# Kernel optimization log

Measured on AMD Instinct MI355X. Metric: run time of the kernel, lower is better.

Reference implementation:

```python
import jax, jax.numpy as jnp
import numpy as np

NS = 33  # segments per image: id 0 = background, 1..32 = objects (fixed max-object count)
EPS_GN = 1e-5


def conv2d(x, w, b, pad):
    y = jax.lax.conv_general_dilated(x, w, window_strides=(1, 1),
                                     padding=[(pad, pad), (pad, pad)],
                                     dimension_numbers=('NCHW', 'OIHW', 'NCHW'))
    return y + b[None, :, None, None]


def group_norm(x, gamma, beta, groups):
    B, C, H, W = x.shape
    xg = x.reshape(B, groups, C // groups, H, W)
    mu = xg.mean((2, 3, 4), keepdims=True)
    var = xg.var((2, 3, 4), keepdims=True)
    xn = ((xg - mu) / jnp.sqrt(var + EPS_GN)).reshape(B, C, H, W)
    return xn * gamma[None, :, None, None] + beta[None, :, None, None]


def setup_inputs() -> dict:
    key = jax.random.key(0)
    ks = jax.random.split(key, 10)
    B, Cf, H, W = 4, 512, 128, 128
    std = 0.01
    inp = {
        'x': jax.random.normal(ks[0], (B, Cf, H, W), jnp.float32),
        'masks': jax.random.randint(ks[1], (B, H, W), 0, NS).astype(jnp.int32),
        # coord_conv: Conv2d(2, 64, 1)
        'w_coord': jax.random.normal(ks[2], (64, 2, 1, 1), jnp.float32) * std,
        'b_coord': jnp.zeros((64,), jnp.float32),
        # encoder convs + groupnorms
        'w1': jax.random.normal(ks[3], (256, Cf + 64, 3, 3), jnp.float32) * std,
        'b1': jnp.zeros((256,), jnp.float32),
        'g1': jnp.ones((256,), jnp.float32), 'bt1': jnp.zeros((256,), jnp.float32),
        'w2': jax.random.normal(ks[4], (128, 256, 3, 3), jnp.float32) * std,
        'b2': jnp.zeros((128,), jnp.float32),
        'g2': jnp.ones((128,), jnp.float32), 'bt2': jnp.zeros((128,), jnp.float32),
        'w3': jax.random.normal(ks[5], (64, 128, 3, 3), jnp.float32) * std,
        'b3': jnp.zeros((64,), jnp.float32),
        'g3': jnp.ones((64,), jnp.float32), 'bt3': jnp.zeros((64,), jnp.float32),
        # heads (1x1 convs on pooled [64] vectors == tiny matmuls)
        'w_box': jax.random.normal(ks[6], (7, 64, 1, 1), jnp.float32) * std,
        'b_box': jnp.zeros((7,), jnp.float32),
        'w_conf': jax.random.normal(ks[7], (1, 64, 1, 1), jnp.float32) * std,
        'b_conf': jnp.zeros((1,), jnp.float32),
    }
    return inp


def reference(x, masks, w_coord, b_coord, w1, b1, g1, bt1, w2, b2, g2, bt2,
              w3, b3, g3, bt3, w_box, b_box, w_conf, b_conf):
    B, _, H, W = x.shape
    # coordinate grid: channels are [grid_x, grid_y]
    gy, gx = jnp.meshgrid(jnp.arange(H), jnp.arange(W), indexing='ij')
    grid = jnp.stack([gx, gy], axis=0).astype(x.dtype)            # [2,H,W]
    grid = jnp.broadcast_to(grid[None], (B, 2, H, W))
    grid_feats = jax.nn.relu(conv2d(grid, w_coord, b_coord, 0))   # [B,64,H,W]

    h = jnp.concatenate([x, grid_feats], axis=1)                  # [B,576,H,W]
    h = jax.nn.relu(group_norm(conv2d(h, w1, b1, 1), g1, bt1, 8))
    h = jax.nn.relu(group_norm(conv2d(h, w2, b2, 1), g2, bt2, 4))
    h = jax.nn.relu(group_norm(conv2d(h, w3, b3, 1), g3, bt3, 4))  # [B,64,H,W]

    # per-(image, object-id) masked mean pooling via segment_sum
    C = h.shape[1]
    flat = h.transpose(0, 2, 3, 1).reshape(-1, C)                 # [B*H*W, 64]
    seg = (jnp.arange(B, dtype=jnp.int32)[:, None] * NS
           + masks.reshape(B, -1)).reshape(-1)                    # [B*H*W]
    sums = jax.ops.segment_sum(flat, seg, num_segments=B * NS).reshape(B, NS, C)
    counts = jax.ops.segment_sum(jnp.ones_like(seg, jnp.float32), seg,
                                 num_segments=B * NS).reshape(B, NS, 1)
    # drop background segment 0; safe divide matches the <1e-4 skip (empty slots -> 0 pooled)
    pooled = sums[:, 1:] / jnp.maximum(counts[:, 1:], 1e-4)       # [B,32,64]

    boxes = jnp.einsum('boc,kc->bok', pooled, w_box.reshape(7, C)) + b_box   # [B,32,7]
    scores = jnp.einsum('boc,c->bo', pooled, w_conf.reshape(C)) + b_conf[0]  # [B,32]
    return boxes, scores
```

## Files before the change

### kernel.cpp

```cpp
#include <hip/hip_runtime.h>

typedef unsigned short u16;
typedef unsigned int u32;
typedef __bf16 bf16x8 __attribute__((ext_vector_type(8)));
typedef float f32x4 __attribute__((ext_vector_type(4)));

__device__ __forceinline__ u16 f2bf(float f) {
  u32 u = __float_as_uint(f);
  u += 0x7fffu + ((u >> 16) & 1u);
  return (u16)(u >> 16);
}
__device__ __forceinline__ float bf2f(u16 h) {
  return __uint_as_float(((u32)h) << 16);
}

#define GLD_LDS16(g, l)                                                        \
  __builtin_amdgcn_global_load_lds(                                            \
      (__attribute__((address_space(1))) void*)(g),                            \
      (__attribute__((address_space(3))) void*)(l), 16, 0, 0)

__global__ __launch_bounds__(256) void prep_k(
    float* smallb, u16* in1, u16* in2, u16* in3, const float* __restrict__ w1,
    u16* __restrict__ wp1, const float* __restrict__ w2, u16* __restrict__ wp2,
    const float* __restrict__ w3, u16* __restrict__ wp3,
    const float* __restrict__ x, const float* __restrict__ wcd,
    const float* __restrict__ bcd) {
  const int bid = blockIdx.x;
  const int t = threadIdx.x;
  __shared__ u16 tile[128 * 65];
  __shared__ float swc[128], sbc[64];

  if (bid < 83) {
    if (bid < 35) {
      int i = bid * 256 + t;
      if (i < 8708) smallb[i] = 0.f;
      return;
    }
    u16* buf;
    int C, sub;
    if (bid < 51)      { buf = in1; C = 576; sub = bid - 35; }
    else if (bid < 67) { buf = in2; C = 256; sub = bid - 51; }
    else               { buf = in3; C = 128; sub = bid - 67; }
    int b = sub >> 2, s = sub & 3;
    int npx = (s < 2) ? 130 : 128;
    u32* base = (u32*)(buf + (size_t)b * 130 * 130 * C);
    int C2 = C >> 1;
    int total = npx * C2;
    for (int i = t; i < total; i += 256) {
      int p = i / C2, r = i - p * C2;
      int y, xx;
      if (s == 0)      { y = 0;     xx = p; }
      else if (s == 1) { y = 129;   xx = p; }
      else if (s == 2) { y = p + 1; xx = 0; }
      else             { y = p + 1; xx = 129; }
      base[(y * 130 + xx) * C2 + r] = 0u;
    }
    return;
  }
  if (bid < 6707) {
    int rel = bid - 83;
    const float* src;
    u16* dst;
    int CIN, COUT, total, base;
    if (rel < 5184)      { src = w1; dst = wp1; CIN = 576; COUT = 256; total = 1327104; base = rel; }
    else if (rel < 6336) { src = w2; dst = wp2; CIN = 256; COUT = 128; total = 294912;  base = rel - 5184; }
    else                 { src = w3; dst = wp3; CIN = 128; COUT = 64;  total = 73728;   base = rel - 6336; }
    int idx = base * 256 + t;
    if (idx >= total) return;
    int kc = idx & 31;
    int n = (idx >> 5) % COUT;
    int q = idx / (32 * COUT);
    int dydx = q % 9, cb = q / 9;
    dst[idx] = f2bf(src[((size_t)n * CIN + cb * 32 + kc) * 9 + dydx]);
    return;
  }
  const int tb = bid - 6707;
  const int b = tb >> 8, h = (tb >> 1) & 127, half = tb & 1;
  const int w0 = half * 64;
  if (t < 128) swc[t] = wcd[t];
  else if (t < 192) sbc[t - 128] = bcd[t - 128];
  const int w = t & 63;
  const int cg = t >> 6;
  const float* xb = x + (((size_t)b * 512) * 128 + h) * 128 + w0 + w;
  u16* ob = in1 + ((size_t)(b * 130 + h + 1) * 130 + (w0 + 1)) * 576;
#pragma unroll 1
  for (int cc = 0; cc < 4; ++cc) {
    const int c0 = cc * 128;
#pragma unroll
    for (int j = 0; j < 32; ++j) {
      int cl = j * 4 + cg;
      tile[cl * 65 + w] = f2bf(xb[(size_t)(c0 + cl) * 16384]);
    }
    __syncthreads();
#pragma unroll
    for (int k = 0; k < 4; ++k) {
      int idx = k * 256 + t;
      int ww = idx >> 4, c8 = (idx & 15) * 8;
      union { uint4 u; u16 s[8]; } o;
#pragma unroll
      for (int i = 0; i < 8; ++i) o.s[i] = tile[(c8 + i) * 65 + ww];
      *(uint4*)(ob + (size_t)ww * 576 + c0 + c8) = o.u;
    }
    __syncthreads();
  }
  const int px = t >> 2, cq = (t & 3) * 16;
  const float fw = (float)(w0 + px), fh = (float)h;
  u16* gp = ob + (size_t)px * 576 + 512 + cq;
#pragma unroll
  for (int j = 0; j < 2; ++j) {
    union { uint4 u; u16 s[8]; } o;
#pragma unroll
    for (int i = 0; i < 8; ++i) {
      int c = cq + j * 8 + i;
      float v = swc[2 * c] * fw + swc[2 * c + 1] * fh + sbc[c];
      o.s[i] = f2bf(fmaxf(v, 0.f));
    }
    *(uint4*)(gp + j * 8) = o.u;
  }
}

template <int CIN, int COUT, int BN, bool NORM>
__global__ __launch_bounds__(256) void conv3x3_k(
    const u16* __restrict__ in, const u16* __restrict__ wp,
    const float* __restrict__ bias, u16* __restrict__ out, int Hp, int Wp,
    int opy, int opx, float* __restrict__ stats, int gsLog2, int nG,
    const float* __restrict__ inStats, const float* __restrict__ inGamma,
    const float* __restrict__ inBeta, int inGsLog2, int inNG) {
  constexpr int CB = CIN / 32;
  constexpr int WN = BN / 2;
  constexpr int NT = WN / 16;
  constexpr int ROWCH = 520;
  constexpr int NCH = 3 * ROWCH;
  constexpr int BUFE = 3 * 130 * 32;
  static_assert(BN == 128 || BN == 64, "");
  __shared__ u16 As3[2 * BUFE];
  __shared__ float redS[8], redQ[8];
  __shared__ float la[NORM ? CIN : 1], lb[NORM ? CIN : 1];

  const int t = threadIdx.x;
  const int L = gridDim.x;
  const int work = (blockIdx.x & 7) * (L >> 3) + (blockIdx.x >> 3);
  const int xt = work >> 9;
  const int rem = work & 511;
  const int b = rem >> 7, h = rem & 127;
  const int n0 = xt * BN;

  const int lane = t & 63, wv = t >> 6;
  const int wm = wv & 1, wn = wv >> 1;
  const int ln = lane & 15, lq = lane >> 4;

  if (t < 8) { redS[t] = 0.f; redQ[t] = 0.f; }
  if (NORM) {
    const float invCnt = 1.f / (16384.f * 32.f);
    for (int i = t; i < CIN; i += 256) {
      int g = i >> inGsLog2;
      float mean = inStats[b * inNG + g] * invCnt;
      float m2 = inStats[4 * inNG + b * inNG + g] * invCnt;
      float rstd = rsqrtf(m2 - mean * mean + 1e-5f);
      float a = inGamma[i] * rstd;
      la[i] = a;
      lb[i] = inBeta[i] - mean * a;
    }
  }

  f32x4 acc[4][NT];
  const f32x4 zero = {0.f, 0.f, 0.f, 0.f};
#pragma unroll
  for (int i = 0; i < 4; ++i)
#pragma unroll
    for (int j = 0; j < NT; ++j) acc[i][j] = zero;

  const u16* inb = in + ((size_t)b * 130 + h) * 130 * CIN;

  int sc[7], srp[7], sqs[7], hz[7];
#pragma unroll
  for (int it = 0; it < 7; ++it) {
    int c = it * 256 + t;
    sc[it] = (c < NCH) ? c : -1;
    int r = (c >= 2 * ROWCH) ? 2 : (c >= ROWCH ? 1 : 0);
    int wch = c - r * ROWCH;
    int pxi = wch >> 2, q = wch & 3;
    srp[it] = (r * 130 + pxi) * CIN + (q ^ ((pxi >> 1) & 3)) * 8;
    sqs[it] = c * 8;
    hz[it] = (pxi == 0) || (pxi == 129) || (r == 0 && h == 0) ||
             (r == 2 && h == 127);
  }

  auto stage = [&](int cb, int sel) {
    const u16* slab = inb + cb * 32;
    u16* dst = &As3[sel * BUFE];
#pragma unroll
    for (int it = 0; it < 7; ++it)
      if (sc[it] >= 0) GLD_LDS16(slab + srp[it], dst + sqs[it]);
  };

  stage(0, 0);

  const u16* wbase0 = wp + ((size_t)n0 + wn * WN + ln) * 32 + lq * 8;

#pragma unroll 1
  for (int cb = 0; cb < CB; ++cb) {
    __syncthreads();
    const int cur = cb & 1;
    const u16* wcb = wbase0 + (size_t)(cb * 9) * COUT * 32;
    u16* Asw = &As3[cur * BUFE];

    bf16x8 fb[NT], fbn[NT];
#pragma unroll
    for (int j = 0; j < NT; ++j) fb[j] = *(const bf16x8*)(wcb + j * 512);

    if (NORM) {
#pragma unroll
      for (int it = 0; it < 7; ++it) {
        if (sc[it] < 0) continue;
        uint4* p = (uint4*)&Asw[sqs[it]];
        if (hz[it]) {
          *p = (uint4){0u, 0u, 0u, 0u};
        } else {
          int chb = cb * 32 + (srp[it] & 31);
          union { uint4 u; u16 s[8]; } d;
          d.u = *p;
#pragma unroll
          for (int e = 0; e < 8; ++e) {
            float v = la[chb + e] * bf2f(d.s[e]) + lb[chb + e];
            d.s[e] = f2bf(fmaxf(v, 0.f));
          }
          *p = d.u;
        }
      }
      __syncthreads();
    }

    if (cb + 1 < CB) stage(cb + 1, 1 - cur);

    bf16x8 fa[4], fan[4];
#pragma unroll
    for (int i = 0; i < 4; ++i) {
      int pxl = wm * 64 + i * 16 + ln;
      int qs = lq ^ ((pxl >> 1) & 3);
      fa[i] = *(const bf16x8*)&Asw[(pxl << 5) + qs * 8];
    }
#pragma unroll
    for (int dydx = 0; dydx < 9; ++dydx) {
      if (dydx < 8) {
        const int dyn = (dydx + 1) / 3, dxn = (dydx + 1) % 3;
#pragma unroll
        for (int j = 0; j < NT; ++j)
          fbn[j] = *(const bf16x8*)(wcb + (size_t)(dydx + 1) * COUT * 32 + j * 512);
#pragma unroll
        for (int i = 0; i < 4; ++i) {
          int pxl = dxn + wm * 64 + i * 16 + ln;
          int qs = lq ^ ((pxl >> 1) & 3);
          fan[i] = *(const bf16x8*)&Asw[((dyn * 130 + pxl) << 5) + qs * 8];
        }
      }
#pragma unroll
      for (int i = 0; i < 4; ++i)
#pragma unroll
        for (int j = 0; j < NT; ++j)
          acc[i][j] = __builtin_amdgcn_mfma_f32_16x16x32_bf16(fa[i], fb[j],
                                                              acc[i][j], 0, 0, 0);
#pragma unroll
      for (int j = 0; j < NT; ++j) fb[j] = fbn[j];
#pragma unroll
      for (int i = 0; i < 4; ++i) fa[i] = fan[i];
    }
  }

#pragma unroll
  for (int j = 0; j < NT; ++j) {
    const int n = n0 + wn * WN + j * 16 + ln;
    const float bv = bias[n];
    float sj = 0.f, qj = 0.f;
#pragma unroll
    for (int i = 0; i < 4; ++i) {
#pragma unroll
      for (int r = 0; r < 4; ++r) {
        const int w = wm * 64 + i * 16 + lq * 4 + r;
        u16 st = f2bf(acc[i][j][r] + bv);
        out[((size_t)(b * Hp + h + opy) * Wp + (w + opx)) * COUT + n] = st;
        float vq = bf2f(st);
        sj += vq;
        qj += vq * vq;
      }
    }
    sj += __shfl_xor(sj, 16, 64);
    sj += __shfl_xor(sj, 32, 64);
    qj += __shfl_xor(qj, 16, 64);
    qj += __shfl_xor(qj, 32, 64);
    if (lq == 0) {
      int gl = (wn * WN + j * 16 + ln) >> gsLog2;
      atomicAdd(&redS[gl], sj);
      atomicAdd(&redQ[gl], qj);
    }
  }
  __syncthreads();
  if (t < (BN >> gsLog2)) {
    int g = (n0 >> gsLog2) + t;
    atomicAdd(&stats[b * nG + g], redS[t]);
    atomicAdd(&stats[4 * nG + b * nG + g], redQ[t]);
  }
}

__global__ __launch_bounds__(256) void pool_k(const u16* __restrict__ h3,
                                              const int* __restrict__ masks,
                                              const float* __restrict__ stats,
                                              const float* __restrict__ gamma,
                                              const float* __restrict__ beta,
                                              float* __restrict__ gsum,
                                              float* __restrict__ gcnt) {
  const int t = threadIdx.x;
  const int b = blockIdx.x >> 6, chunk = blockIdx.x & 63;
  __shared__ float ls[33 * 64];
  __shared__ float lc[33];
  for (int i = t; i < 33 * 64; i += 256) ls[i] = 0.f;
  if (t < 33) lc[t] = 0.f;
  const int c = t & 63;
  const int g = c >> 4;
  const float invCnt = 1.f / (16384.f * 16.f);
  float mean = stats[b * 4 + g] * invCnt;
  float m2 = stats[16 + b * 4 + g] * invCnt;
  float rstd = rsqrtf(m2 - mean * mean + 1e-5f);
  const float a = gamma[c] * rstd;
  const float cc = beta[c] - mean * a;
  __syncthreads();
  const int p0 = chunk * 256;
  for (int i = 0; i < 64; ++i) {
    int p = p0 + i * 4 + (t >> 6);
    int id = masks[b * 16384 + p];
    float v = bf2f(h3[((size_t)b * 16384 + p) * 64 + c]);
    v = fmaxf(a * v + cc, 0.f);
    atomicAdd(&ls[id * 64 + c], v);
    if (c == 0) atomicAdd(&lc[id], 1.f);
  }
  __syncthreads();
  for (int i = t; i < 33 * 64; i += 256) atomicAdd(&gsum[b * 2112 + i], ls[i]);
  if (t < 33) atomicAdd(&gcnt[b * 33 + t], lc[t]);
}

__global__ __launch_bounds__(256) void heads_k(const float* __restrict__ gsum,
                                               const float* __restrict__ gcnt,
                                               const float* __restrict__ wbox,
                                               const float* __restrict__ bbox,
                                               const float* __restrict__ wconf,
                                               const float* __restrict__ bconf,
                                               float* __restrict__ out) {
  int idx = blockIdx.x * 256 + threadIdx.x;
  if (idx >= 1024) return;
  if (idx < 896) {
    int b = idx / 224, r = idx % 224;
    int o = r / 7, k = r % 7;
    float inv = 1.f / fmaxf(gcnt[b * 33 + o + 1], 1e-4f);
    const float* ps = gsum + (b * 33 + o + 1) * 64;
    float s = 0.f;
    for (int c = 0; c < 64; ++c) s += ps[c] * wbox[k * 64 + c];
    out[idx] = s * inv + bbox[k];
  } else {
    int i = idx - 896;
    int b = i >> 5, o = i & 31;
    float inv = 1.f / fmaxf(gcnt[b * 33 + o + 1], 1e-4f);
    const float* ps = gsum + (b * 33 + o + 1) * 64;
    float s = 0.f;
    for (int c = 0; c < 64; ++c) s += ps[c] * wconf[c];
    out[896 + i] = s * inv + bconf[0];
  }
}

extern "C" void kernel_launch(void* const* d_in, const int* in_sizes, int n_in,
                              void* d_out, int out_size, void* d_ws,
                              size_t ws_size, hipStream_t stream) {
  (void)in_sizes; (void)n_in; (void)out_size; (void)ws_size;
  const float* x       = (const float*)d_in[0];
  const int*   masks   = (const int*)d_in[1];
  const float* w_coord = (const float*)d_in[2];
  const float* b_coord = (const float*)d_in[3];
  const float* w1  = (const float*)d_in[4];
  const float* b1  = (const float*)d_in[5];
  const float* g1  = (const float*)d_in[6];
  const float* bt1 = (const float*)d_in[7];
  const float* w2  = (const float*)d_in[8];
  const float* b2  = (const float*)d_in[9];
  const float* g2  = (const float*)d_in[10];
  const float* bt2 = (const float*)d_in[11];
  const float* w3  = (const float*)d_in[12];
  const float* b3  = (const float*)d_in[13];
  const float* g3  = (const float*)d_in[14];
  const float* bt3 = (const float*)d_in[15];
  const float* wbox  = (const float*)d_in[16];
  const float* bbox  = (const float*)d_in[17];
  const float* wconf = (const float*)d_in[18];
  const float* bconf = (const float*)d_in[19];
  float* out = (float*)d_out;

  char* ws = (char*)d_ws;
  size_t off = 0;
  auto take = [&](size_t bytes) {
    size_t o = off;
    off += (bytes + 255) & ~(size_t)255;
    return o;
  };
  u16* in1 = (u16*)(ws + take((size_t)4 * 130 * 130 * 576 * 2));
  u16* in2 = (u16*)(ws + take((size_t)4 * 130 * 130 * 256 * 2));
  u16* in3 = (u16*)(ws + take((size_t)4 * 130 * 130 * 128 * 2));
  u16* wp1 = (u16*)(ws + take((size_t)9 * 576 * 256 * 2));
  u16* wp2 = (u16*)(ws + take((size_t)9 * 256 * 128 * 2));
  u16* wp3 = (u16*)(ws + take((size_t)9 * 128 * 64 * 2));
  float* smallb = (float*)(ws + take(8708 * 4));
  u16* h3 = in1;

  float* s1   = smallb;
  float* s2   = smallb + 64;
  float* s3   = smallb + 96;
  float* psum = smallb + 128;
  float* pcnt = smallb + 8576;

  prep_k<<<dim3(7731), 256, 0, stream>>>(smallb, in1, in2, in3, w1, wp1, w2,
                                         wp2, w3, wp3, x, w_coord, b_coord);

  conv3x3_k<576, 256, 128, false><<<dim3(1024), 256, 0, stream>>>(
      in1, wp1, b1, in2, 130, 130, 1, 1, s1, 5, 8, nullptr, nullptr, nullptr, 0, 0);

  conv3x3_k<256, 128, 128, true><<<dim3(512), 256, 0, stream>>>(
      in2, wp2, b2, in3, 130, 130, 1, 1, s2, 5, 4, s1, g1, bt1, 5, 8);

  conv3x3_k<128, 64, 64, true><<<dim3(512), 256, 0, stream>>>(
      in3, wp3, b3, h3, 128, 128, 0, 0, s3, 4, 4, s2, g2, bt2, 5, 4);

  pool_k<<<dim3(256), 256, 0, stream>>>(h3, masks, s3, g3, bt3, psum, pcnt);
  heads_k<<<dim3(4), 256, 0, stream>>>(psum, pcnt, wbox, bbox, wconf, bconf, out);
}
```

Baseline: 561.9 us.

## Compute two output rows per conv block to reuse staged input rows

Each conv3x3 block now produces two adjacent output rows instead of one. It stages four input rows (instead of three) into LDS and assigns one wave row to each output row, so the staged input and the weight fragments are shared across both rows. This cuts the input staging traffic per output and halves the grid size. In exchange the LDS footprint grows, accumulators double to 8xNT per wave, staging addresses are recomputed each iteration instead of precomputed, and a launch-bounds occupancy hint of 2 is added. The grid is now 512/256 blocks, which may leave CUs underfilled.

New measurement: 629.8 us. +12.1%, slower.

```diff
diff --git a/kernel.cpp b/kernel.cpp
--- a/kernel.cpp
+++ b/kernel.cpp
@@ -120,7 +120,7 @@
 }
 
 template <int CIN, int COUT, int BN, bool NORM>
-__global__ __launch_bounds__(256) void conv3x3_k(
+__global__ __launch_bounds__(256, 2) void conv3x3_k(
     const u16* __restrict__ in, const u16* __restrict__ wp,
     const float* __restrict__ bias, u16* __restrict__ out, int Hp, int Wp,
     int opy, int opx, float* __restrict__ stats, int gsLog2, int nG,
@@ -130,8 +130,8 @@
   constexpr int WN = BN / 2;
   constexpr int NT = WN / 16;
   constexpr int ROWCH = 520;
-  constexpr int NCH = 3 * ROWCH;
-  constexpr int BUFE = 3 * 130 * 32;
+  constexpr int NCH = 4 * ROWCH;
+  constexpr int BUFE = 4 * 130 * 32;
   static_assert(BN == 128 || BN == 64, "");
   __shared__ u16 As3[2 * BUFE];
   __shared__ float redS[8], redQ[8];
@@ -140,9 +140,10 @@
   const int t = threadIdx.x;
   const int L = gridDim.x;
   const int work = (blockIdx.x & 7) * (L >> 3) + (blockIdx.x >> 3);
-  const int xt = work >> 9;
-  const int rem = work & 511;
-  const int b = rem >> 7, h = rem & 127;
+  const int xt = work >> 8;
+  const int rem = work & 255;
+  const int b = rem >> 6, rp = rem & 63;
+  const int h0 = rp * 2;
   const int n0 = xt * BN;
 
   const int lane = t & 63, wv = t >> 6;
@@ -163,35 +164,29 @@
     }
   }
 
-  f32x4 acc[4][NT];
+  f32x4 acc[8][NT];
   const f32x4 zero = {0.f, 0.f, 0.f, 0.f};
 #pragma unroll
-  for (int i = 0; i < 4; ++i)
+  for (int i = 0; i < 8; ++i)
 #pragma unroll
     for (int j = 0; j < NT; ++j) acc[i][j] = zero;
 
-  const u16* inb = in + ((size_t)b * 130 + h) * 130 * CIN;
-
-  int sc[7], srp[7], sqs[7], hz[7];
-#pragma unroll
-  for (int it = 0; it < 7; ++it) {
-    int c = it * 256 + t;
-    sc[it] = (c < NCH) ? c : -1;
-    int r = (c >= 2 * ROWCH) ? 2 : (c >= ROWCH ? 1 : 0);
-    int wch = c - r * ROWCH;
-    int pxi = wch >> 2, q = wch & 3;
-    srp[it] = (r * 130 + pxi) * CIN + (q ^ ((pxi >> 1) & 3)) * 8;
-    sqs[it] = c * 8;
-    hz[it] = (pxi == 0) || (pxi == 129) || (r == 0 && h == 0) ||
-             (r == 2 && h == 127);
-  }
+  const u16* inb = in + ((size_t)b * 130 + h0) * 130 * CIN;
 
   auto stage = [&](int cb, int sel) {
     const u16* slab = inb + cb * 32;
     u16* dst = &As3[sel * BUFE];
 #pragma unroll
-    for (int it = 0; it < 7; ++it)
-      if (sc[it] >= 0) GLD_LDS16(slab + srp[it], dst + sqs[it]);
+    for (int it = 0; it < 9; ++it) {
+      int c = it * 256 + t;
+      if (c < NCH) {
+        int r = c / ROWCH;
+        int wch = c - r * ROWCH;
+        int pxi = wch >> 2, q = wch & 3;
+        int qs = q ^ ((pxi >> 1) & 3);
+        GLD_LDS16(slab + (r * 130 + pxi) * CIN + qs * 8, dst + c * 8);
+      }
+    }
   };
 
   stage(0, 0);
@@ -211,13 +206,19 @@
 
     if (NORM) {
 #pragma unroll
-      for (int it = 0; it < 7; ++it) {
-        if (sc[it] < 0) continue;
-        uint4* p = (uint4*)&Asw[sqs[it]];
-        if (hz[it]) {
+      for (int it = 0; it < 9; ++it) {
+        int c = it * 256 + t;
+        if (c >= NCH) continue;
+        int r = c / ROWCH;
+        int wch = c - r * ROWCH;
+        int pxi = wch >> 2, q = wch & 3;
+        int qs = q ^ ((pxi >> 1) & 3);
+        uint4* p = (uint4*)&Asw[c * 8];
+        bool halo = (pxi == 0) || (pxi == 129) || (h0 + r == 0) || (h0 + r == 129);
+        if (halo) {
           *p = (uint4){0u, 0u, 0u, 0u};
         } else {
-          int chb = cb * 32 + (srp[it] & 31);
+          int chb = cb * 32 + qs * 8;
           union { uint4 u; u16 s[8]; } d;
           d.u = *p;
 #pragma unroll
@@ -233,37 +234,27 @@
 
     if (cb + 1 < CB) stage(cb + 1, 1 - cur);
 
-    bf16x8 fa[4], fan[4];
-#pragma unroll
-    for (int i = 0; i < 4; ++i) {
-      int pxl = wm * 64 + i * 16 + ln;
-      int qs = lq ^ ((pxl >> 1) & 3);
-      fa[i] = *(const bf16x8*)&Asw[(pxl << 5) + qs * 8];
-    }
 #pragma unroll
     for (int dydx = 0; dydx < 9; ++dydx) {
+      const int dy = dydx / 3, dx = dydx % 3;
       if (dydx < 8) {
-        const int dyn = (dydx + 1) / 3, dxn = (dydx + 1) % 3;
 #pragma unroll
         for (int j = 0; j < NT; ++j)
           fbn[j] = *(const bf16x8*)(wcb + (size_t)(dydx + 1) * COUT * 32 + j * 512);
-#pragma unroll
-        for (int i = 0; i < 4; ++i) {
-          int pxl = dxn + wm * 64 + i * 16 + ln;
-          int qs = lq ^ ((pxl >> 1) & 3);
-          fan[i] = *(const bf16x8*)&Asw[((dyn * 130 + pxl) << 5) + qs * 8];
-        }
       }
-#pragma unroll
-      for (int i = 0; i < 4; ++i)
+      const int row = wm + dy;
+#pragma unroll
+      for (int i = 0; i < 8; ++i) {
+        int pxl = dx + i * 16 + ln;
+        int qs = lq ^ ((pxl >> 1) & 3);
+        bf16x8 fa = *(const bf16x8*)&Asw[((row * 130 + pxl) << 5) + qs * 8];
 #pragma unroll
         for (int j = 0; j < NT; ++j)
-          acc[i][j] = __builtin_amdgcn_mfma_f32_16x16x32_bf16(fa[i], fb[j],
+          acc[i][j] = __builtin_amdgcn_mfma_f32_16x16x32_bf16(fa, fb[j],
                                                               acc[i][j], 0, 0, 0);
+      }
 #pragma unroll
       for (int j = 0; j < NT; ++j) fb[j] = fbn[j];
-#pragma unroll
-      for (int i = 0; i < 4; ++i) fa[i] = fan[i];
     }
   }
 
@@ -273,12 +264,12 @@
     const float bv = bias[n];
     float sj = 0.f, qj = 0.f;
 #pragma unroll
-    for (int i = 0; i < 4; ++i) {
+    for (int i = 0; i < 8; ++i) {
 #pragma unroll
       for (int r = 0; r < 4; ++r) {
-        const int w = wm * 64 + i * 16 + lq * 4 + r;
+        const int w = i * 16 + lq * 4 + r;
         u16 st = f2bf(acc[i][j][r] + bv);
-        out[((size_t)(b * Hp + h + opy) * Wp + (w + opx)) * COUT + n] = st;
+        out[((size_t)(b * Hp + h0 + wm + opy) * Wp + (w + opx)) * COUT + n] = st;
         float vq = bf2f(st);
         sj += vq;
         qj += vq * vq;
@@ -417,13 +408,13 @@
   prep_k<<<dim3(7731), 256, 0, stream>>>(smallb, in1, in2, in3, w1, wp1, w2,
                                          wp2, w3, wp3, x, w_coord, b_coord);
 
-  conv3x3_k<576, 256, 128, false><<<dim3(1024), 256, 0, stream>>>(
+  conv3x3_k<576, 256, 128, false><<<dim3(512), 256, 0, stream>>>(
       in1, wp1, b1, in2, 130, 130, 1, 1, s1, 5, 8, nullptr, nullptr, nullptr, 0, 0);
 
-  conv3x3_k<256, 128, 128, true><<<dim3(512), 256, 0, stream>>>(
+  conv3x3_k<256, 128, 128, true><<<dim3(256), 256, 0, stream>>>(
       in2, wp2, b2, in3, 130, 130, 1, 1, s2, 5, 4, s1, g1, bt1, 5, 8);
 
-  conv3x3_k<128, 64, 64, true><<<dim3(512), 256, 0, stream>>>(
+  conv3x3_k<128, 64, 64, true><<<dim3(256), 256, 0, stream>>>(
       in3, wp3, b3, h3, 128, 128, 0, 0, s3, 4, 4, s2, g2, bt2, 5, 4);
 
   pool_k<<<dim3(256), 256, 0, stream>>>(h3, masks, s3, g3, bt3, psum, pcnt);
```
